# Performance work log

Measured on AMD Instinct MI355X. Metric: run time of the kernel, lower is better.

The kernel has to match this reference:

```python
import jax, jax.numpy as jnp
import numpy as np

N, E = 3072, 49152
C_IN, HID, C_OUT = 16, 64, 3
KS = (2000, 1000, 500)  # ceil(pool_ratio * n_nodes) per depth: 2000/3072, 0.5, 0.5


def gcn(x, A, W, b):
    # GCNConv(improved=True) with edge weights: A_hat = A + 2I,
    # out = D^-1/2 A_hat D^-1/2 (x W) + b
    n = A.shape[0]
    i = jnp.arange(n)
    A_hat = A.at[i, i].add(2.0)
    deg = A_hat.sum(axis=1)
    dis = jnp.where(deg > 0, 1.0 / jnp.sqrt(deg), 0.0)
    return (dis[:, None] * A_hat * dis[None, :]) @ (x @ W) + b


def augment(A):
    # GraphUNet.augment_adj: remove self loops, add self loops (w=1),
    # spspmm(A, A) -> A^2, remove self loops. Dense equivalent.
    n = A.shape[0]
    i = jnp.arange(n)
    A1 = A.at[i, i].set(1.0)
    A2 = A1 @ A1
    return A2.at[i, i].set(0.0)


def topk_pool(x, A, p, k):
    # TopKPooling: score = tanh((x . p)/||p||), keep top-k nodes, scale features
    score = jnp.tanh((x @ p) / jnp.linalg.norm(p))
    _, perm = jax.lax.top_k(score, k)
    x = x[perm] * score[perm][:, None]
    return x, A[perm][:, perm], perm


def setup_inputs():
    key = jax.random.key(0)
    ks = jax.random.split(key, 16)
    g = lambda k, shape, s=1.0: jax.random.normal(k, shape, dtype=jnp.float32) * s
    s = 0.1
    return {
        "x": g(ks[0], (N, C_IN)),
        "edge_index": jax.random.randint(ks[1], (2, E), 0, N),
        "Wd0": g(ks[2], (C_IN, HID), s), "bd0": jnp.zeros((HID,), jnp.float32),
        "Wd1": g(ks[3], (HID, HID), s), "bd1": jnp.zeros((HID,), jnp.float32),
        "Wd2": g(ks[4], (HID, HID), s), "bd2": jnp.zeros((HID,), jnp.float32),
        "Wd3": g(ks[5], (HID, HID), s), "bd3": jnp.zeros((HID,), jnp.float32),
        "p1": g(ks[6], (HID,), s), "p2": g(ks[7], (HID,), s), "p3": g(ks[8], (HID,), s),
        "Wu0": g(ks[9], (HID, HID), s), "bu0": jnp.zeros((HID,), jnp.float32),
        "Wu1": g(ks[10], (HID, HID), s), "bu1": jnp.zeros((HID,), jnp.float32),
        "Wu2": g(ks[11], (HID, C_OUT), s), "bu2": jnp.zeros((C_OUT,), jnp.float32),
    }


def reference(x, edge_index, Wd0, bd0, Wd1, bd1, Wd2, bd2, Wd3, bd3,
              p1, p2, p3, Wu0, bu0, Wu1, bu1, Wu2, bu2):
    # eval mode: dropout_edge(p=0.2) and F.dropout(p=0.92) are identity
    # dense weighted adjacency; duplicate edges sum, matching sparse scatter-add
    A = jnp.zeros((N, N), jnp.float32).at[edge_index[0], edge_index[1]].add(1.0)
    x = jax.nn.relu(gcn(x, A, Wd0, bd0))
    xs, adjs, perms = [x], [A], []
    for i, (W, b, p) in enumerate(((Wd1, bd1, p1), (Wd2, bd2, p2), (Wd3, bd3, p3))):
        A = augment(A)
        x, A, perm = topk_pool(x, A, p, KS[i])
        x = jax.nn.relu(gcn(x, A, W, b))
        if i < 2:
            xs.append(x)
            adjs.append(A)
        perms.append(perm)
    for i, (W, b) in enumerate(((Wu0, bu0), (Wu1, bu1), (Wu2, bu2))):
        j = 2 - i
        res, Aj, perm = xs[j], adjs[j], perms[j]
        up = jnp.zeros_like(res).at[perm].set(x)  # unpool
        x = gcn(res + up, Aj, W, b)  # sum_res=True skip connection
        if i < 2:
            x = jax.nn.relu(x)
    return jax.nn.softmax(x, axis=1)
```

## Files before the change

### kernel.cpp

```cpp
#include <hip/hip_runtime.h>
#include <hip/hip_bf16.h>
#include <cstdint>
#include <cstddef>
#include <math.h>


#define DIVUP(a,b) (((a)+(b)-1)/(b))

using s16x8 = __attribute__((ext_vector_type(8))) short;
using f32x4 = __attribute__((ext_vector_type(4))) float;

template<int N> __device__ __forceinline__ void waitvm() {
    if constexpr (N == 0)       asm volatile("s_waitcnt vmcnt(0)" ::: "memory");
    else if constexpr (N == 4)  asm volatile("s_waitcnt vmcnt(4)" ::: "memory");
    else if constexpr (N == 8)  asm volatile("s_waitcnt vmcnt(8)" ::: "memory");
    else                        asm volatile("s_waitcnt vmcnt(16)" ::: "memory");
}

__device__ __forceinline__ unsigned short f2bf(float v) {
    union { float f; unsigned u; } a; a.f = v;
    unsigned u = a.u;
    u = u + 0x7FFFu + ((u >> 16) & 1u);
    return (unsigned short)(u >> 16);
}
__device__ __forceinline__ float bf2f(unsigned short h) {
    union { unsigned u; float f; } a; a.u = ((unsigned)h) << 16; return a.f;
}
__device__ __forceinline__ unsigned char f2e4m3(float v) {
    if (v <= 0.f) return 0;
    int e = 0; float m = v;
    while (m >= 2.f) { m *= 0.5f; ++e; }
    int mant = (int)(m * 8.f + 0.5f) - 8;
    if (mant >= 8) { mant = 0; ++e; }
    return (unsigned char)(((e + 7) << 3) | mant);
}
__device__ __forceinline__ void gload_lds16(const unsigned short* g, unsigned short* l) {
    __builtin_amdgcn_global_load_lds(
        (const __attribute__((address_space(1))) void*)g,
        (__attribute__((address_space(3))) void*)l, 16, 0, 0);
}
__device__ __forceinline__ void gload_lds16b(const unsigned char* g, unsigned char* l) {
    __builtin_amdgcn_global_load_lds(
        (const __attribute__((address_space(1))) void*)g,
        (__attribute__((address_space(3))) void*)l, 16, 0, 0);
}


__global__ void k_scatter(const int* __restrict__ e, float* __restrict__ A, int E, int n) {
    int t = blockIdx.x * blockDim.x + threadIdx.x;
    if (t < E) atomicAdd(&A[(size_t)e[t] * n + e[E + t]], 1.0f);
}

__global__ void k_a0_plane(const float* __restrict__ A, unsigned short* __restrict__ H,
                           unsigned char* __restrict__ F8,
                           float* __restrict__ d0, float* __restrict__ dsum, int n) {
    int t = blockIdx.x * 256 + threadIdx.x;
    int i = t / n, j = t - i * n;
    float v = A[t];
    if (i == j) { d0[i] = v; v = 1.0f; }
    H[t] = f2bf(v);
    F8[t] = f2e4m3(v);
    __shared__ float red[256];
    red[threadIdx.x] = v; __syncthreads();
    for (int o = 128; o > 0; o >>= 1) {
        if (threadIdx.x < o) red[threadIdx.x] += red[threadIdx.x + o];
        __syncthreads();
    }
    if (threadIdx.x == 0) atomicAdd(&dsum[i], red[0]);
}

__global__ void k_transpose_u8(const unsigned char* __restrict__ S, unsigned char* __restrict__ D, int n) {
    __shared__ unsigned char tile[32][33];
    int bx = blockIdx.x * 32, by = blockIdx.y * 32;
    #pragma unroll
    for (int dy = 0; dy < 32; dy += 8)
        tile[threadIdx.y + dy][threadIdx.x] = S[(size_t)(by + threadIdx.y + dy) * n + bx + threadIdx.x];
    __syncthreads();
    #pragma unroll
    for (int dy = 0; dy < 32; dy += 8)
        D[(size_t)(bx + threadIdx.y + dy) * n + by + threadIdx.x] = tile[threadIdx.x][threadIdx.y + dy];
}

__global__ void k_disv(const float* __restrict__ dsum, const float* __restrict__ diag,
                       float* __restrict__ dis, int n) {
    int i = blockIdx.x * blockDim.x + threadIdx.x;
    if (i >= n) return;
    float deg = dsum[i] + 1.0f + (diag ? diag[i] : 0.0f);
    dis[i] = deg > 0.f ? 1.0f / sqrtf(deg) : 0.f;
}

__global__ void k_disp(const unsigned short* __restrict__ P0, const unsigned short* __restrict__ P1,
                       const unsigned short* __restrict__ P2, int nplanes,
                       float* __restrict__ dis, int np) {
    int i = blockIdx.x;
    const unsigned short* pls[3] = {P0, P1, P2};
    float s = 0.f;
    for (int p = 0; p < nplanes; ++p) {
        const unsigned short* row = pls[p] + (size_t)i * np;
        for (int j = threadIdx.x * 8; j < np; j += 2048) {
            s16x8 v = *(const s16x8*)(row + j);
            #pragma unroll
            for (int e = 0; e < 8; ++e) s += bf2f((unsigned short)v[e]);
        }
    }
    __shared__ float red[256];
    red[threadIdx.x] = s; __syncthreads();
    for (int o = 128; o > 0; o >>= 1) {
        if (threadIdx.x < o) red[threadIdx.x] += red[threadIdx.x + o];
        __syncthreads();
    }
    if (threadIdx.x == 0) dis[i] = 1.0f / sqrtf(red[0] + 1.0f);
}

__global__ void k_scores(const float* __restrict__ x, const float* __restrict__ pv,
                         float* __restrict__ sc, int n) {
    __shared__ float pl[64];
    if (threadIdx.x < 64) pl[threadIdx.x] = pv[threadIdx.x];
    __syncthreads();
    float n2 = 0.f;
    #pragma unroll
    for (int k = 0; k < 64; ++k) n2 += pl[k] * pl[k];
    float nrm = sqrtf(n2);
    int i = blockIdx.x * blockDim.x + threadIdx.x;
    if (i >= n) return;
    const float* xr = x + (size_t)i * 64;
    float d = 0.f;
    #pragma unroll
    for (int k = 0; k < 64; ++k) d += xr[k] * pl[k];
    sc[i] = tanhf(d / nrm);
}

__global__ void k_count_rank(const float* __restrict__ score, int* __restrict__ rank, int n) {
    __shared__ float ls[256];
    const int i = blockIdx.x * 256 + threadIdx.x;
    const int j0 = blockIdx.y * 256;
    int jj_n = n - j0; if (jj_n > 256) jj_n = 256;
    ls[threadIdx.x] = (j0 + threadIdx.x < n) ? score[j0 + threadIdx.x] : -INFINITY;
    __syncthreads();
    if (i >= n) return;
    const float si = score[i];
    int cnt = 0;
    for (int jj = 0; jj < jj_n; ++jj) {
        float sj = ls[jj];
        int j = j0 + jj;
        cnt += (sj > si) || (sj == si && j < i);
    }
    atomicAdd(&rank[i], cnt);
}

__global__ void k_topk_finish(const float* __restrict__ score, const int* __restrict__ rank,
                              const float* __restrict__ x, int n, int k, int kp,
                              int* __restrict__ perm, float* __restrict__ scout,
                              float* __restrict__ xo) {
    int i = blockIdx.x * blockDim.x + threadIdx.x;
    if (i < n) {
        int r = rank[i];
        if (r < k) {
            float s = score[i];
            perm[r] = i; scout[r] = s;
            const float* xr = x + (size_t)i * 64;
            float* xw = xo + (size_t)r * 64;
            #pragma unroll 8
            for (int f = 0; f < 64; ++f) xw[f] = xr[f] * s;
        }
    }
    if (i >= k && i < kp) { perm[i] = 0; scout[i] = 0.f; }
}

__global__ void k_unpool(const float* __restrict__ res, const float* __restrict__ xc,
                         const int* __restrict__ rank, float* __restrict__ o, int n, int k) {
    int t = blockIdx.x * blockDim.x + threadIdx.x;
    if (t >= n * 64) return;
    int r = rank[t >> 6];
    o[t] = res[t] + (r < k ? xc[(size_t)r * 64 + (t & 63)] : 0.f);
}

__global__ void k_xw(const float* __restrict__ x, const float* __restrict__ W,
                     const float* __restrict__ dis, int n, int np, int cin, int ldw, int nout,
                     float* __restrict__ Y, unsigned short* __restrict__ T0,
                     unsigned short* __restrict__ T1, unsigned short* __restrict__ T2) {
    int t = blockIdx.x * blockDim.x + threadIdx.x;
    if (t >= np * 64) return;
    int i = t >> 6, f = t & 63;
    float y = 0.f;
    if (i < n && f < nout) {
        float a = 0.f;
        for (int k = 0; k < cin; ++k) a += x[(size_t)i * cin + k] * W[(size_t)k * ldw + f];
        y = dis[i] * a;
    }
    Y[t] = y;
    unsigned short h0 = f2bf(y);
    float r1 = y - bf2f(h0);
    unsigned short h1 = f2bf(r1);
    float r2 = r1 - bf2f(h1);
    size_t ti = (size_t)f * np + i;
    T0[ti] = h0; T1[ti] = h1; T2[ti] = f2bf(r2);
}


__global__ __launch_bounds__(256) void k_aug8(
    const unsigned char* __restrict__ P8, const unsigned char* __restrict__ Q8,
    const int* __restrict__ perm, int kk, int kp, int K, int ns,
    unsigned short* __restrict__ H0, unsigned short* __restrict__ T0)
{
    constexpr int BM = 128;
    constexpr int PS = 128 * 64;
    constexpr int D = 3;
    constexpr int STG = 2 * PS;
    constexpr int SMEB = (D * STG > 128 * 130 * 2) ? D * STG : 128 * 130 * 2;
    __shared__ __align__(16) unsigned char smem[SMEB];
    const int tid = threadIdx.x, lane = tid & 63;
    const int wm = tid >> 7, wn = (tid >> 6) & 1;
    const int bm = blockIdx.x * BM, bn = blockIdx.y * BM;
    const unsigned char* spA[2];
    const unsigned char* spB[2];
    int dstb[2];
    #pragma unroll
    for (int it = 0; it < 2; ++it) {
        int s = tid + it * 256;
        int row = s >> 2, c = (s & 3) ^ (row & 3);
        dstb[it] = (s - lane) * 16;
        spA[it] = P8 + (size_t)perm[bm + row] * ns + 16 * c;
        spB[it] = Q8 + (size_t)perm[bn + row] * ns + 16 * c;
    }
    f32x4 acc[4][4] = {};
    const int l15 = lane & 15, kb = lane >> 4;
    const int nt = K >> 6;

    auto stage = [&](int b, int koff) {
        unsigned char* base = smem + b * STG;
        #pragma unroll
        for (int it = 0; it < 2; ++it) gload_lds16b(spA[it] + koff, base + dstb[it]);
        #pragma unroll
        for (int it = 0; it < 2; ++it) gload_lds16b(spB[it] + koff, base + PS + dstb[it]);
    };
    auto compute = [&](int b) {
        const unsigned char* base = smem + b * STG;
        #pragma unroll
        for (int h = 0; h < 2; ++h) {
            long av[4], bv[4];
            #pragma unroll
            for (int mi = 0; mi < 4; ++mi) {
                int row = wm * 64 + mi * 16 + l15;
                int slot = (h * 2 + (kb >> 1)) ^ (row & 3);
                av[mi] = *(const long*)(base + row * 64 + slot * 16 + (kb & 1) * 8);
            }
            #pragma unroll
            for (int ni = 0; ni < 4; ++ni) {
                int row = wn * 64 + ni * 16 + l15;
                int slot = (h * 2 + (kb >> 1)) ^ (row & 3);
                bv[ni] = *(const long*)(base + PS + row * 64 + slot * 16 + (kb & 1) * 8);
            }
            #pragma unroll
            for (int mi = 0; mi < 4; ++mi)
                #pragma unroll
                for (int ni = 0; ni < 4; ++ni)
                    acc[mi][ni] = __builtin_amdgcn_mfma_f32_16x16x32_fp8_fp8(
                        av[mi], bv[ni], acc[mi][ni], 0, 0, 0);
        }
    };

    stage(0, 0); stage(1, 64);
    for (int t = 0; t < nt; ++t) {
        const int ahead = nt - 1 - t;
        if (ahead >= D - 1) {
            stage((t + D - 1) % D, (t + D - 1) * 64);
            waitvm<8>();
        } else if (ahead == 1) {
            waitvm<4>();
        } else {
            waitvm<0>();
        }
        __builtin_amdgcn_sched_barrier(0);
        __builtin_amdgcn_s_barrier();
        compute(t % D);
        __builtin_amdgcn_s_barrier();
    }

    const int hi = lane >> 4;
    #pragma unroll
    for (int mi = 0; mi < 4; ++mi)
        #pragma unroll
        for (int ni = 0; ni < 4; ++ni)
            #pragma unroll
            for (int r = 0; r < 4; ++r) {
                int row = bm + wm * 64 + mi * 16 + hi * 4 + r;
                int col = bn + wn * 64 + ni * 16 + l15;
                float v = (row < kk && col < kk) ? ((row == col) ? 1.f : acc[mi][ni][r]) : 0.f;
                H0[(size_t)row * kp + col] = f2bf(v);
            }

    unsigned short* smw = (unsigned short*)smem;
    __syncthreads();
    #pragma unroll
    for (int mi = 0; mi < 4; ++mi)
        #pragma unroll
        for (int ni = 0; ni < 4; ++ni)
            #pragma unroll
            for (int r = 0; r < 4; ++r) {
                int rl = wm * 64 + mi * 16 + hi * 4 + r;
                int cl = wn * 64 + ni * 16 + l15;
                int row = bm + rl, col = bn + cl;
                float v = (row < kk && col < kk) ? ((row == col) ? 1.f : acc[mi][ni][r]) : 0.f;
                smw[rl * 130 + cl] = f2bf(v);
            }
    __syncthreads();
    #pragma unroll
    for (int e = 0; e < 64; ++e) {
        int idx = tid + e * 256;
        int j = idx >> 7, i = idx & 127;
        T0[(size_t)(bn + j) * kp + (bm + i)] = smw[i * 130 + j];
    }
}

template<int TM, int PA, int PB, int NP, int NT>
__global__ __launch_bounds__(256) void k_aug2(
    const unsigned short* __restrict__ Pa, const unsigned short* __restrict__ Pb,
    const unsigned short* __restrict__ Qa, const unsigned short* __restrict__ Qb,
    const int* __restrict__ perm, int kk, int kp, int K, int ns,
    unsigned short* __restrict__ H0, unsigned short* __restrict__ H1,
    unsigned short* __restrict__ H2,
    unsigned short* __restrict__ T0, unsigned short* __restrict__ T1)
{
    constexpr int BM  = TM * 32;
    constexpr int PS  = TM * 2048;
    constexpr int D   = 3;
    constexpr int STG = (PA + PB) * PS;
    constexpr int LPS = TM * (PA + PB);
    constexpr int TRE = NT ? (BM * (BM + 2)) : 0;
    constexpr int SME = (D * STG > TRE) ? (D * STG) : TRE;
    __shared__ __align__(16) unsigned short smem[SME];
    const int tid = threadIdx.x, lane = tid & 63;
    const int wm = tid >> 7, wn = (tid >> 6) & 1;
    const int bm = blockIdx.x * BM, bn = blockIdx.y * BM;
    const unsigned short* P[2] = {Pa, Pb};
    const unsigned short* Q[2] = {Qa, Qb};
    const unsigned short* sp[PA][TM];
    const unsigned short* sq[PB][TM];
    int dst[TM];
    #pragma unroll
    for (int it = 0; it < TM; ++it) {
        int s = tid + it * 256;
        int row = s >> 3, c = (s & 7) ^ (row & 7);
        dst[it] = (s - lane) * 8;
        #pragma unroll
        for (int p = 0; p < PA; ++p)
            sp[p][it] = P[p] + (size_t)perm[bm + row] * ns + 8 * c;
        #pragma unroll
        for (int p = 0; p < PB; ++p)
            sq[p][it] = Q[p] + (size_t)perm[bn + row] * ns + 8 * c;
    }
    f32x4 acc[TM][TM] = {};
    const int l15 = lane & 15, kb = lane >> 4;
    const int nt = K >> 6;

    auto stage = [&](int b, int koff) {
        unsigned short* base = smem + b * STG;
        #pragma unroll
        for (int p = 0; p < PA; ++p)
            #pragma unroll
            for (int it = 0; it < TM; ++it)
                gload_lds16(sp[p][it] + koff, base + p * PS + dst[it]);
        #pragma unroll
        for (int p = 0; p < PB; ++p)
            #pragma unroll
            for (int it = 0; it < TM; ++it)
                gload_lds16(sq[p][it] + koff, base + PA * PS + p * PS + dst[it]);
    };
    auto compute = [&](int b) {
        const unsigned short* base = smem + b * STG;
        #pragma unroll
        for (int h = 0; h < 2; ++h) {
            s16x8 av[PA][TM], bv[PB][TM];
            #pragma unroll
            for (int p = 0; p < PA; ++p)
                #pragma unroll
                for (int mi = 0; mi < TM; ++mi) {
                    int row = wm * (TM * 16) + mi * 16 + l15;
                    int slot = (h * 4 + kb) ^ (row & 7);
                    av[p][mi] = *(const s16x8*)(base + p * PS + row * 64 + slot * 8);
                }
            #pragma unroll
            for (int p = 0; p < PB; ++p)
                #pragma unroll
                for (int ni = 0; ni < TM; ++ni) {
                    int row = wn * (TM * 16) + ni * 16 + l15;
                    int slot = (h * 4 + kb) ^ (row & 7);
                    bv[p][ni] = *(const s16x8*)(base + PA * PS + p * PS + row * 64 + slot * 8);
                }
            #pragma unroll
            for (int mi = 0; mi < TM; ++mi)
                #pragma unroll
                for (int ni = 0; ni < TM; ++ni)
                    #pragma unroll
                    for (int pa = 0; pa < PA; ++pa)
                        #pragma unroll
                        for (int pb = 0; pb < PB; ++pb)
                            acc[mi][ni] = __builtin_amdgcn_mfma_f32_16x16x32_bf16(
                                av[pa][mi], bv[pb][ni], acc[mi][ni], 0, 0, 0);
        }
    };

    for (int i = 0; i < D - 1; ++i) stage(i, i * 64);
    for (int t = 0; t < nt; ++t) {
        const int ahead = nt - 1 - t;
        if (ahead >= D - 1) {
            stage((t + D - 1) % D, (t + D - 1) * 64);
            waitvm<2 * LPS>();
        } else if (ahead == 1) {
            waitvm<LPS>();
        } else {
            waitvm<0>();
        }
        __builtin_amdgcn_sched_barrier(0);
        __builtin_amdgcn_s_barrier();
        compute(t % D);
        __builtin_amdgcn_s_barrier();
    }

    const int hi = lane >> 4;
    #pragma unroll
    for (int mi = 0; mi < TM; ++mi)
        #pragma unroll
        for (int ni = 0; ni < TM; ++ni)
            #pragma unroll
            for (int r = 0; r < 4; ++r) {
                int row = bm + wm * (TM * 16) + mi * 16 + hi * 4 + r;
                int col = bn + wn * (TM * 16) + ni * 16 + l15;
                float v = (row < kk && col < kk) ? ((row == col) ? 1.f : acc[mi][ni][r]) : 0.f;
                unsigned short h0 = f2bf(v);
                size_t o = (size_t)row * kp + col;
                H0[o] = h0;
                if (NP > 1) {
                    float r1 = v - bf2f(h0);
                    unsigned short h1 = f2bf(r1);
                    H1[o] = h1;
                    if (NP > 2) H2[o] = f2bf(r1 - bf2f(h1));
                }
            }

    if (NT > 0) {
        #pragma unroll
        for (int pass = 0; pass < NT; ++pass) {
            __syncthreads();
            #pragma unroll
            for (int mi = 0; mi < TM; ++mi)
                #pragma unroll
                for (int ni = 0; ni < TM; ++ni)
                    #pragma unroll
                    for (int r = 0; r < 4; ++r) {
                        int rl = wm * (TM * 16) + mi * 16 + hi * 4 + r;
                        int cl = wn * (TM * 16) + ni * 16 + l15;
                        int row = bm + rl, col = bn + cl;
                        float v = (row < kk && col < kk) ? ((row == col) ? 1.f : acc[mi][ni][r]) : 0.f;
                        unsigned short h0 = f2bf(v);
                        unsigned short hv = h0;
                        if (pass == 1) hv = f2bf(v - bf2f(h0));
                        smem[rl * (BM + 2) + cl] = hv;
                    }
            __syncthreads();
            unsigned short* T = pass ? T1 : T0;
            #pragma unroll
            for (int e = 0; e < BM * BM / 256; ++e) {
                int idx = tid + e * 256;
                int j = idx / BM, i = idx & (BM - 1);
                T[(size_t)(bn + j) * kp + (bm + i)] = smem[i * (BM + 2) + j];
            }
        }
    }
}

template<int PA>
__global__ __launch_bounds__(256) void k_gcn_gemm(
    const unsigned short* __restrict__ Aa, const unsigned short* __restrict__ Ab,
    const unsigned short* __restrict__ Ac,
    const unsigned short* __restrict__ B0, const unsigned short* __restrict__ B1,
    const unsigned short* __restrict__ B2,
    int np, int kchunk, float* __restrict__ Zp)
{
    __shared__ __align__(16) unsigned short la[PA * 4096];
    __shared__ __align__(16) unsigned short lb[3 * 4096];
    const int tid = threadIdx.x, lane = tid & 63, wv = tid >> 6;
    const int bm = blockIdx.x * 64;
    const int kbeg = blockIdx.y * kchunk;
    const unsigned short* A[3] = {Aa, Ab, Ac};
    const unsigned short* B[3] = {B0, B1, B2};
    const unsigned short* sa[PA][2];
    const unsigned short* sb[3][2];
    int dst[2];
    #pragma unroll
    for (int it = 0; it < 2; ++it) {
        int s = tid + it * 256;
        int row = s >> 3, c = (s & 7) ^ (row & 7);
        dst[it] = (s - lane) * 8;
        #pragma unroll
        for (int p = 0; p < PA; ++p)
            sa[p][it] = A[p] + (size_t)(bm + row) * np + kbeg + 8 * c;
        #pragma unroll
        for (int p = 0; p < 3; ++p)
            sb[p][it] = B[p] + (size_t)row * np + kbeg + 8 * c;
    }
    f32x4 acc[4] = {};
    const int l15 = lane & 15, kb = lane >> 4;
    const int nt = kchunk >> 6;

    for (int tt = 0; tt < nt; ++tt) {
        if (tt) __syncthreads();
        int koff = tt * 64;
        #pragma unroll
        for (int p = 0; p < PA; ++p)
            #pragma unroll
            for (int it = 0; it < 2; ++it)
                gload_lds16(sa[p][it] + koff, &la[p * 4096 + dst[it]]);
        #pragma unroll
        for (int p = 0; p < 3; ++p)
            #pragma unroll
            for (int it = 0; it < 2; ++it)
                gload_lds16(sb[p][it] + koff, &lb[p * 4096 + dst[it]]);
        __syncthreads();
        #pragma unroll
        for (int h = 0; h < 2; ++h) {
            s16x8 av[PA], bv[3][4];
            #pragma unroll
            for (int p = 0; p < PA; ++p) {
                int row = wv * 16 + l15;
                int slot = (h * 4 + kb) ^ (row & 7);
                av[p] = *(const s16x8*)&la[p * 4096 + row * 64 + slot * 8];
            }
            #pragma unroll
            for (int p = 0; p < 3; ++p)
                #pragma unroll
                for (int ni = 0; ni < 4; ++ni) {
                    int row = ni * 16 + l15;
                    int slot = (h * 4 + kb) ^ (row & 7);
                    bv[p][ni] = *(const s16x8*)&lb[p * 4096 + row * 64 + slot * 8];
                }
            #pragma unroll
            for (int ni = 0; ni < 4; ++ni)
                #pragma unroll
                for (int pa = 0; pa < PA; ++pa)
                    #pragma unroll
                    for (int pb = 0; pb <= 2 - pa; ++pb)
                        acc[ni] = __builtin_amdgcn_mfma_f32_16x16x32_bf16(
                            av[pa], bv[pb][ni], acc[ni], 0, 0, 0);
        }
    }

    const int l4 = lane >> 4;
    float* Z = Zp + (size_t)blockIdx.y * np * 64;
    for (int ni = 0; ni < 4; ++ni)
        #pragma unroll
        for (int r = 0; r < 4; ++r) {
            int row = bm + wv * 16 + l4 * 4 + r;
            Z[(size_t)row * 64 + ni * 16 + l15] = acc[ni][r];
        }
}

__global__ void k_gcn_epi(const float* __restrict__ Zp, const float* __restrict__ Y,
                          const float* __restrict__ dis, const float* __restrict__ diagv,
                          const float* __restrict__ b, int n, int np, int nout, int relu,
                          int S, float* __restrict__ xo) {
    int t = blockIdx.x * blockDim.x + threadIdx.x;
    if (t >= n * 64) return;
    int i = t >> 6, f = t & 63;
    float s = 0.f;
    for (int kq = 0; kq < S; ++kq) s += Zp[(size_t)kq * np * 64 + t];
    float coef = 1.f + (diagv ? diagv[i] : 0.f);
    float v = dis[i] * (s + coef * Y[t]) + (f < nout ? b[f] : 0.f);
    if (relu) v = fmaxf(v, 0.f);
    xo[t] = v;
}

__global__ void k_softmax(const float* __restrict__ lg, float* __restrict__ o, int n) {
    int i = blockIdx.x * blockDim.x + threadIdx.x;
    if (i >= n) return;
    float a = lg[i * 64], b = lg[i * 64 + 1], c = lg[i * 64 + 2];
    float m = fmaxf(a, fmaxf(b, c));
    float ea = expf(a - m), eb = expf(b - m), ec = expf(c - m);
    float s = ea + eb + ec;
    o[i * 3] = ea / s; o[i * 3 + 1] = eb / s; o[i * 3 + 2] = ec / s;
}


extern "C" void kernel_launch(void* const* d_in, const int* in_sizes, int n_in,
                              void* d_out, int out_size, void* d_ws, size_t ws_size,
                              hipStream_t stream) {
    const int N0 = 3072;
    const int E = in_sizes[1] / 2;
    const int CIN = in_sizes[0] / N0;

    const float* x_in = (const float*)d_in[0];
    const int*   eidx = (const int*)d_in[1];
    const float* Wd0 = (const float*)d_in[2];  const float* bd0 = (const float*)d_in[3];
    const float* Wd1 = (const float*)d_in[4];  const float* bd1 = (const float*)d_in[5];
    const float* Wd2 = (const float*)d_in[6];  const float* bd2 = (const float*)d_in[7];
    const float* Wd3 = (const float*)d_in[8];  const float* bd3 = (const float*)d_in[9];
    const float* p1  = (const float*)d_in[10]; const float* p2  = (const float*)d_in[11];
    const float* p3  = (const float*)d_in[12];
    const float* Wu0 = (const float*)d_in[13]; const float* bu0 = (const float*)d_in[14];
    const float* Wu1 = (const float*)d_in[15]; const float* bu1 = (const float*)d_in[16];
    const float* Wu2 = (const float*)d_in[17]; const float* bu2 = (const float*)d_in[18];
    float* out = (float*)d_out;

    char* ws = (char*)d_ws;
    size_t off = 0;
    auto alloc = [&](size_t bytes) -> void* {
        off = (off + 255) & ~(size_t)255;
        void* p = ws + off;
        off += bytes;
        return p;
    };

    unsigned short* A0H  = (unsigned short*)alloc((size_t)3072 * 3072 * 2);
    unsigned char*  A0F8 = (unsigned char*)alloc((size_t)3072 * 3072);
    unsigned char*  A0T8 = (unsigned char*)alloc((size_t)3072 * 3072);
    float* d0   = (float*)alloc(3072 * 4);
    float* dis0 = (float*)alloc(3072 * 4);
    float* x0   = (float*)alloc((size_t)3072 * 64 * 4);
    unsigned short* P1H = (unsigned short*)alloc((size_t)2048 * 2048 * 2);
    unsigned short* P1T = (unsigned short*)alloc((size_t)2048 * 2048 * 2);
    float* dis1 = (float*)alloc(2048 * 4);
    float* x1   = (float*)alloc((size_t)2048 * 64 * 4);
    float* xp1  = (float*)alloc((size_t)2048 * 64 * 4);
    unsigned short* P2H  = (unsigned short*)alloc((size_t)1024 * 1024 * 2);
    unsigned short* P2L  = (unsigned short*)alloc((size_t)1024 * 1024 * 2);
    unsigned short* P2TH = (unsigned short*)alloc((size_t)1024 * 1024 * 2);
    unsigned short* P2TL = (unsigned short*)alloc((size_t)1024 * 1024 * 2);
    float* dis2 = (float*)alloc(1024 * 4);
    float* x2   = (float*)alloc((size_t)1024 * 64 * 4);
    float* xp2  = (float*)alloc((size_t)1024 * 64 * 4);
    unsigned short* P3a = (unsigned short*)alloc((size_t)512 * 512 * 2);
    unsigned short* P3b = (unsigned short*)alloc((size_t)512 * 512 * 2);
    unsigned short* P3c = (unsigned short*)alloc((size_t)512 * 512 * 2);
    float* dis3 = (float*)alloc(512 * 4);
    float* x3   = (float*)alloc((size_t)512 * 64 * 4);
    float* xp3  = (float*)alloc((size_t)512 * 64 * 4);
    int*   perm1 = (int*)alloc(2048 * 4);  float* sc1 = (float*)alloc(2048 * 4);
    int*   perm2 = (int*)alloc(1024 * 4);  float* sc2 = (float*)alloc(1024 * 4);
    int*   perm3 = (int*)alloc(512 * 4);   float* sc3 = (float*)alloc(512 * 4);
    float* score = (float*)alloc(3072 * 4);
    float* dsum0 = (float*)alloc(3072 * 4);
    int* rank1 = (int*)alloc(3072 * 4);
    int* rank2 = (int*)alloc(2048 * 4);
    int* rank3 = (int*)alloc(1024 * 4);
    float* Yf  = (float*)alloc((size_t)3072 * 64 * 4);
    unsigned short* Yt0 = (unsigned short*)alloc((size_t)64 * 3072 * 2);
    unsigned short* Yt1 = (unsigned short*)alloc((size_t)64 * 3072 * 2);
    unsigned short* Yt2 = (unsigned short*)alloc((size_t)64 * 3072 * 2);
    float* Zp   = (float*)alloc((size_t)8 * 3072 * 64 * 4);
    float* xlog = (float*)alloc((size_t)3072 * 64 * 4);
    float* t2b  = (float*)alloc((size_t)1024 * 64 * 4);
    float* t1b  = (float*)alloc((size_t)2048 * 64 * 4);
    float* t0b  = (float*)alloc((size_t)3072 * 64 * 4);
    char* scratch = (char*)alloc((size_t)3072 * 3072 * 4);
    if (off > ws_size) return;

    float* A0f = (float*)scratch;

    auto gcn = [&](const float* xin, int cin, const float* W, int ldw, int nout, const float* bias,
                   const unsigned short* Pa, const unsigned short* Pb2, const unsigned short* Pc,
                   int PA, int n, int np2, const float* dis, const float* diagv, int relu, float* xout) {
        k_xw<<<DIVUP(np2 * 64, 256), 256, 0, stream>>>(xin, W, dis, n, np2, cin, ldw, nout, Yf, Yt0, Yt1, Yt2);
        int S = (np2 == 1024) ? 16 : 8;
        int kch = np2 / S;
        dim3 gg(np2 / 64, S);
        if (PA == 1)      k_gcn_gemm<1><<<gg, 256, 0, stream>>>(Pa, Pa, Pa, Yt0, Yt1, Yt2, np2, kch, Zp);
        else if (PA == 2) k_gcn_gemm<2><<<gg, 256, 0, stream>>>(Pa, Pb2, Pb2, Yt0, Yt1, Yt2, np2, kch, Zp);
        else              k_gcn_gemm<3><<<gg, 256, 0, stream>>>(Pa, Pb2, Pc, Yt0, Yt1, Yt2, np2, kch, Zp);
        k_gcn_epi<<<DIVUP(n * 64, 256), 256, 0, stream>>>(Zp, Yf, dis, diagv, bias, n, np2, nout, relu, S, xout);
    };

    auto topk = [&](const float* x, const float* pvec, int n, int k, int kp,
                    int* rank, int* perm, float* scv, float* xo) {
        k_scores<<<DIVUP(n, 256), 256, 0, stream>>>(x, pvec, score, n);
        dim3 gr(DIVUP(n, 256), DIVUP(n, 256));
        k_count_rank<<<gr, 256, 0, stream>>>(score, rank, n);
        k_topk_finish<<<DIVUP(n, 256), 256, 0, stream>>>(score, rank, x, n, k, kp, perm, scv, xo);
    };

    hipMemsetAsync(dsum0, 0, (char*)(rank3 + 1024) - (char*)dsum0, stream);

    hipMemsetAsync(A0f, 0, (size_t)3072 * 3072 * 4, stream);
    k_scatter<<<DIVUP(E, 256), 256, 0, stream>>>(eidx, A0f, E, N0);
    k_a0_plane<<<3072 * 3072 / 256, 256, 0, stream>>>(A0f, A0H, A0F8, d0, dsum0, N0);
    k_transpose_u8<<<dim3(96, 96), dim3(32, 8), 0, stream>>>(A0F8, A0T8, 3072);
    k_disv<<<DIVUP(3072, 256), 256, 0, stream>>>(dsum0, d0, dis0, 3072);

    gcn(x_in, CIN, Wd0, 64, 64, bd0, A0H, A0H, A0H, 1, 3072, 3072, dis0, d0, 1, x0);

    topk(x0, p1, 3072, 2000, 2048, rank1, perm1, sc1, xp1);
    k_aug8<<<dim3(16, 16), 256, 0, stream>>>(
        A0F8, A0T8, perm1, 2000, 2048, 3072, 3072, P1H, P1T);
    k_disp<<<2000, 256, 0, stream>>>(P1H, P1H, P1H, 1, dis1, 2048);
    gcn(xp1, 64, Wd1, 64, 64, bd1, P1H, P1H, P1H, 1, 2000, 2048, dis1, nullptr, 1, x1);

    topk(x1, p2, 2000, 1000, 1024, rank2, perm2, sc2, xp2);
    k_aug2<2, 1, 1, 2, 2><<<dim3(16, 16), 256, 0, stream>>>(
        P1H, P1H, P1T, P1T, perm2, 1000, 1024, 2048, 2048, P2H, P2L, P2L, P2TH, P2TL);
    k_disp<<<1000, 256, 0, stream>>>(P2H, P2L, P2L, 2, dis2, 1024);
    gcn(xp2, 64, Wd2, 64, 64, bd2, P2H, P2L, P2L, 2, 1000, 1024, dis2, nullptr, 1, x2);

    topk(x2, p3, 1000, 500, 512, rank3, perm3, sc3, xp3);
    k_aug2<2, 2, 2, 3, 0><<<dim3(8, 8), 256, 0, stream>>>(
        P2H, P2L, P2TH, P2TL, perm3, 500, 512, 1024, 1024, P3a, P3b, P3c, nullptr, nullptr);
    k_disp<<<500, 256, 0, stream>>>(P3a, P3b, P3c, 3, dis3, 512);
    gcn(xp3, 64, Wd3, 64, 64, bd3, P3a, P3b, P3c, 3, 500, 512, dis3, nullptr, 1, x3);

    k_unpool<<<DIVUP(1000 * 64, 256), 256, 0, stream>>>(x2, x3, rank3, t2b, 1000, 500);
    gcn(t2b, 64, Wu0, 64, 64, bu0, P2H, P2L, P2L, 2, 1000, 1024, dis2, nullptr, 1, xp2);

    k_unpool<<<DIVUP(2000 * 64, 256), 256, 0, stream>>>(x1, xp2, rank2, t1b, 2000, 1000);
    gcn(t1b, 64, Wu1, 64, 64, bu1, P1H, P1H, P1H, 1, 2000, 2048, dis1, nullptr, 1, xp1);

    k_unpool<<<DIVUP(3072 * 64, 256), 256, 0, stream>>>(x0, xp1, rank1, t0b, 3072, 2000);
    gcn(t0b, 64, Wu2, 3, 3, bu2, A0H, A0H, A0H, 1, 3072, 3072, dis0, d0, 0, xlog);

    k_softmax<<<DIVUP(3072, 256), 256, 0, stream>>>(xlog, out, 3072);
}
```

Baseline: 405.8 us.

## Fuse degree sums into augment epilogues and permute fp8 layout for wide LDS reads

The augment GEMM epilogues now reduce each output row across lanes and atomically add it into a per-level degree buffer. This replaces the separate k_disp kernels, which reread the pooled bf16 planes, with the cheap k_disv. The fp8 adjacency and its transpose are stored with a 64-column permutation, so the fp8 GEMM loads one 16-byte vector per row per k-tile instead of two 8-byte loads. The swizzle is adjusted to match, and the transpose now uses 64x64 tiles. Degrees are now summed from unrounded float values, a small numerical change, and the epilogue adds shuffle and atomic work.

```diff
diff --git a/kernel.cpp b/kernel.cpp
--- a/kernel.cpp
+++ b/kernel.cpp
@@ -9,6 +9,7 @@
 
 using s16x8 = __attribute__((ext_vector_type(8))) short;
 using f32x4 = __attribute__((ext_vector_type(4))) float;
+using l64x2 = __attribute__((ext_vector_type(2))) long;
 
 template<int N> __device__ __forceinline__ void waitvm() {
     if constexpr (N == 0)       asm volatile("s_waitcnt vmcnt(0)" ::: "memory");
@@ -33,6 +34,9 @@
     int mant = (int)(m * 8.f + 0.5f) - 8;
     if (mant >= 8) { mant = 0; ++e; }
     return (unsigned char)(((e + 7) << 3) | mant);
+}
+__device__ __forceinline__ int perm64(int x) {
+    return ((x >> 3) & 3) * 16 + ((x >> 5) & 1) * 8 + (x & 7);
 }
 __device__ __forceinline__ void gload_lds16(const unsigned short* g, unsigned short* l) {
     __builtin_amdgcn_global_load_lds(
@@ -59,7 +63,7 @@
     float v = A[t];
     if (i == j) { d0[i] = v; v = 1.0f; }
     H[t] = f2bf(v);
-    F8[t] = f2e4m3(v);
+    F8[(size_t)i * n + (j & ~63) + perm64(j & 63)] = f2e4m3(v);
     __shared__ float red[256];
     red[threadIdx.x] = v; __syncthreads();
     for (int o = 128; o > 0; o >>= 1) {
@@ -69,16 +73,17 @@
     if (threadIdx.x == 0) atomicAdd(&dsum[i], red[0]);
 }
 
-__global__ void k_transpose_u8(const unsigned char* __restrict__ S, unsigned char* __restrict__ D, int n) {
-    __shared__ unsigned char tile[32][33];
-    int bx = blockIdx.x * 32, by = blockIdx.y * 32;
-    #pragma unroll
-    for (int dy = 0; dy < 32; dy += 8)
-        tile[threadIdx.y + dy][threadIdx.x] = S[(size_t)(by + threadIdx.y + dy) * n + bx + threadIdx.x];
+__global__ void k_transpose_i8(const unsigned char* __restrict__ S, unsigned char* __restrict__ D, int n) {
+    __shared__ unsigned char tile[64][65];
+    int bx = blockIdx.x * 64, by = blockIdx.y * 64;
+    const int tx = threadIdx.x & 63, ty = threadIdx.x >> 6;
+    #pragma unroll
+    for (int dy = 0; dy < 64; dy += 4)
+        tile[ty + dy][tx] = S[(size_t)(by + ty + dy) * n + bx + perm64(tx)];
     __syncthreads();
     #pragma unroll
-    for (int dy = 0; dy < 32; dy += 8)
-        D[(size_t)(bx + threadIdx.y + dy) * n + by + threadIdx.x] = tile[threadIdx.x][threadIdx.y + dy];
+    for (int dy = 0; dy < 64; dy += 4)
+        D[(size_t)(bx + ty + dy) * n + by + perm64(tx)] = tile[tx][ty + dy];
 }
 
 __global__ void k_disv(const float* __restrict__ dsum, const float* __restrict__ diag,
@@ -87,29 +92,6 @@
     if (i >= n) return;
     float deg = dsum[i] + 1.0f + (diag ? diag[i] : 0.0f);
     dis[i] = deg > 0.f ? 1.0f / sqrtf(deg) : 0.f;
-}
-
-__global__ void k_disp(const unsigned short* __restrict__ P0, const unsigned short* __restrict__ P1,
-                       const unsigned short* __restrict__ P2, int nplanes,
-                       float* __restrict__ dis, int np) {
-    int i = blockIdx.x;
-    const unsigned short* pls[3] = {P0, P1, P2};
-    float s = 0.f;
-    for (int p = 0; p < nplanes; ++p) {
-        const unsigned short* row = pls[p] + (size_t)i * np;
-        for (int j = threadIdx.x * 8; j < np; j += 2048) {
-            s16x8 v = *(const s16x8*)(row + j);
-            #pragma unroll
-            for (int e = 0; e < 8; ++e) s += bf2f((unsigned short)v[e]);
-        }
-    }
-    __shared__ float red[256];
-    red[threadIdx.x] = s; __syncthreads();
-    for (int o = 128; o > 0; o >>= 1) {
-        if (threadIdx.x < o) red[threadIdx.x] += red[threadIdx.x + o];
-        __syncthreads();
-    }
-    if (threadIdx.x == 0) dis[i] = 1.0f / sqrtf(red[0] + 1.0f);
 }
 
 __global__ void k_scores(const float* __restrict__ x, const float* __restrict__ pv,
@@ -201,9 +183,9 @@
 __global__ __launch_bounds__(256) void k_aug8(
     const unsigned char* __restrict__ P8, const unsigned char* __restrict__ Q8,
     const int* __restrict__ perm, int kk, int kp, int K, int ns,
-    unsigned short* __restrict__ H0, unsigned short* __restrict__ T0)
+    unsigned short* __restrict__ H0, unsigned short* __restrict__ T0,
+    float* __restrict__ dsum)
 {
-    constexpr int BM = 128;
     constexpr int PS = 128 * 64;
     constexpr int D = 3;
     constexpr int STG = 2 * PS;
@@ -211,14 +193,14 @@
     __shared__ __align__(16) unsigned char smem[SMEB];
     const int tid = threadIdx.x, lane = tid & 63;
     const int wm = tid >> 7, wn = (tid >> 6) & 1;
-    const int bm = blockIdx.x * BM, bn = blockIdx.y * BM;
+    const int bm = blockIdx.x * 128, bn = blockIdx.y * 128;
     const unsigned char* spA[2];
     const unsigned char* spB[2];
     int dstb[2];
     #pragma unroll
     for (int it = 0; it < 2; ++it) {
         int s = tid + it * 256;
-        int row = s >> 2, c = (s & 3) ^ (row & 3);
+        int row = s >> 2, c = (s & 3) ^ ((row >> 1) & 3);
         dstb[it] = (s - lane) * 16;
         spA[it] = P8 + (size_t)perm[bm + row] * ns + 16 * c;
         spB[it] = Q8 + (size_t)perm[bn + row] * ns + 16 * c;
@@ -236,28 +218,27 @@
     };
     auto compute = [&](int b) {
         const unsigned char* base = smem + b * STG;
-        #pragma unroll
-        for (int h = 0; h < 2; ++h) {
-            long av[4], bv[4];
-            #pragma unroll
-            for (int mi = 0; mi < 4; ++mi) {
-                int row = wm * 64 + mi * 16 + l15;
-                int slot = (h * 2 + (kb >> 1)) ^ (row & 3);
-                av[mi] = *(const long*)(base + row * 64 + slot * 16 + (kb & 1) * 8);
-            }
-            #pragma unroll
-            for (int ni = 0; ni < 4; ++ni) {
-                int row = wn * 64 + ni * 16 + l15;
-                int slot = (h * 2 + (kb >> 1)) ^ (row & 3);
-                bv[ni] = *(const long*)(base + PS + row * 64 + slot * 16 + (kb & 1) * 8);
-            }
+        l64x2 av[4], bv[4];
+        #pragma unroll
+        for (int mi = 0; mi < 4; ++mi) {
+            int row = wm * 64 + mi * 16 + l15;
+            int slot = kb ^ ((row >> 1) & 3);
+            av[mi] = *(const l64x2*)(base + row * 64 + slot * 16);
+        }
+        #pragma unroll
+        for (int ni = 0; ni < 4; ++ni) {
+            int row = wn * 64 + ni * 16 + l15;
+            int slot = kb ^ ((row >> 1) & 3);
+            bv[ni] = *(const l64x2*)(base + PS + row * 64 + slot * 16);
+        }
+        #pragma unroll
+        for (int h = 0; h < 2; ++h)
             #pragma unroll
             for (int mi = 0; mi < 4; ++mi)
                 #pragma unroll
                 for (int ni = 0; ni < 4; ++ni)
                     acc[mi][ni] = __builtin_amdgcn_mfma_f32_16x16x32_fp8_fp8(
-                        av[mi], bv[ni], acc[mi][ni], 0, 0, 0);
-        }
+                        av[mi][h], bv[ni][h], acc[mi][ni], 0, 0, 0);
     };
 
     stage(0, 0); stage(1, 64);
@@ -281,14 +262,20 @@
     #pragma unroll
     for (int mi = 0; mi < 4; ++mi)
         #pragma unroll
-        for (int ni = 0; ni < 4; ++ni)
-            #pragma unroll
-            for (int r = 0; r < 4; ++r) {
-                int row = bm + wm * 64 + mi * 16 + hi * 4 + r;
+        for (int r = 0; r < 4; ++r) {
+            int row = bm + wm * 64 + mi * 16 + hi * 4 + r;
+            float s = 0.f;
+            #pragma unroll
+            for (int ni = 0; ni < 4; ++ni) {
                 int col = bn + wn * 64 + ni * 16 + l15;
                 float v = (row < kk && col < kk) ? ((row == col) ? 1.f : acc[mi][ni][r]) : 0.f;
                 H0[(size_t)row * kp + col] = f2bf(v);
+                s += v;
             }
+            #pragma unroll
+            for (int m = 1; m < 16; m <<= 1) s += __shfl_xor(s, m);
+            if (l15 == 0) atomicAdd(&dsum[row], s);
+        }
 
     unsigned short* smw = (unsigned short*)smem;
     __syncthreads();
@@ -320,7 +307,8 @@
     const int* __restrict__ perm, int kk, int kp, int K, int ns,
     unsigned short* __restrict__ H0, unsigned short* __restrict__ H1,
     unsigned short* __restrict__ H2,
-    unsigned short* __restrict__ T0, unsigned short* __restrict__ T1)
+    unsigned short* __restrict__ T0, unsigned short* __restrict__ T1,
+    float* __restrict__ dsum)
 {
     constexpr int BM  = TM * 32;
     constexpr int PS  = TM * 2048;
@@ -422,12 +410,14 @@
     #pragma unroll
     for (int mi = 0; mi < TM; ++mi)
         #pragma unroll
-        for (int ni = 0; ni < TM; ++ni)
-            #pragma unroll
-            for (int r = 0; r < 4; ++r) {
-                int row = bm + wm * (TM * 16) + mi * 16 + hi * 4 + r;
+        for (int r = 0; r < 4; ++r) {
+            int row = bm + wm * (TM * 16) + mi * 16 + hi * 4 + r;
+            float s = 0.f;
+            #pragma unroll
+            for (int ni = 0; ni < TM; ++ni) {
                 int col = bn + wn * (TM * 16) + ni * 16 + l15;
                 float v = (row < kk && col < kk) ? ((row == col) ? 1.f : acc[mi][ni][r]) : 0.f;
+                s += v;
                 unsigned short h0 = f2bf(v);
                 size_t o = (size_t)row * kp + col;
                 H0[o] = h0;
@@ -438,6 +428,10 @@
                     if (NP > 2) H2[o] = f2bf(r1 - bf2f(h1));
                 }
             }
+            #pragma unroll
+            for (int m = 1; m < 16; m <<= 1) s += __shfl_xor(s, m);
+            if (l15 == 0) atomicAdd(&dsum[row], s);
+        }
 
     if (NT > 0) {
         #pragma unroll
@@ -640,6 +634,9 @@
     int*   perm3 = (int*)alloc(512 * 4);   float* sc3 = (float*)alloc(512 * 4);
     float* score = (float*)alloc(3072 * 4);
     float* dsum0 = (float*)alloc(3072 * 4);
+    float* dsum1 = (float*)alloc(2048 * 4);
+    float* dsum2 = (float*)alloc(1024 * 4);
+    float* dsum3 = (float*)alloc(512 * 4);
     int* rank1 = (int*)alloc(3072 * 4);
     int* rank2 = (int*)alloc(2048 * 4);
     int* rank3 = (int*)alloc(1024 * 4);
@@ -683,27 +680,27 @@
     hipMemsetAsync(A0f, 0, (size_t)3072 * 3072 * 4, stream);
     k_scatter<<<DIVUP(E, 256), 256, 0, stream>>>(eidx, A0f, E, N0);
     k_a0_plane<<<3072 * 3072 / 256, 256, 0, stream>>>(A0f, A0H, A0F8, d0, dsum0, N0);
-    k_transpose_u8<<<dim3(96, 96), dim3(32, 8), 0, stream>>>(A0F8, A0T8, 3072);
+    k_transpose_i8<<<dim3(48, 48), 256, 0, stream>>>(A0F8, A0T8, 3072);
     k_disv<<<DIVUP(3072, 256), 256, 0, stream>>>(dsum0, d0, dis0, 3072);
 
     gcn(x_in, CIN, Wd0, 64, 64, bd0, A0H, A0H, A0H, 1, 3072, 3072, dis0, d0, 1, x0);
 
     topk(x0, p1, 3072, 2000, 2048, rank1, perm1, sc1, xp1);
     k_aug8<<<dim3(16, 16), 256, 0, stream>>>(
-        A0F8, A0T8, perm1, 2000, 2048, 3072, 3072, P1H, P1T);
-    k_disp<<<2000, 256, 0, stream>>>(P1H, P1H, P1H, 1, dis1, 2048);
+        A0F8, A0T8, perm1, 2000, 2048, 3072, 3072, P1H, P1T, dsum1);
+    k_disv<<<DIVUP(2048, 256), 256, 0, stream>>>(dsum1, nullptr, dis1, 2048);
     gcn(xp1, 64, Wd1, 64, 64, bd1, P1H, P1H, P1H, 1, 2000, 2048, dis1, nullptr, 1, x1);
 
     topk(x1, p2, 2000, 1000, 1024, rank2, perm2, sc2, xp2);
     k_aug2<2, 1, 1, 2, 2><<<dim3(16, 16), 256, 0, stream>>>(
-        P1H, P1H, P1T, P1T, perm2, 1000, 1024, 2048, 2048, P2H, P2L, P2L, P2TH, P2TL);
-    k_disp<<<1000, 256, 0, stream>>>(P2H, P2L, P2L, 2, dis2, 1024);
+        P1H, P1H, P1T, P1T, perm2, 1000, 1024, 2048, 2048, P2H, P2L, P2L, P2TH, P2TL, dsum2);
+    k_disv<<<DIVUP(1024, 256), 256, 0, stream>>>(dsum2, nullptr, dis2, 1024);
     gcn(xp2, 64, Wd2, 64, 64, bd2, P2H, P2L, P2L, 2, 1000, 1024, dis2, nullptr, 1, x2);
 
     topk(x2, p3, 1000, 500, 512, rank3, perm3, sc3, xp3);
     k_aug2<2, 2, 2, 3, 0><<<dim3(8, 8), 256, 0, stream>>>(
-        P2H, P2L, P2TH, P2TL, perm3, 500, 512, 1024, 1024, P3a, P3b, P3c, nullptr, nullptr);
-    k_disp<<<500, 256, 0, stream>>>(P3a, P3b, P3c, 3, dis3, 512);
+        P2H, P2L, P2TH, P2TL, perm3, 500, 512, 1024, 1024, P3a, P3b, P3c, nullptr, nullptr, dsum3);
+    k_disv<<<DIVUP(512, 256), 256, 0, stream>>>(dsum3, nullptr, dis3, 512);
     gcn(xp3, 64, Wd3, 64, 64, bd3, P3a, P3b, P3c, 3, 500, 512, dis3, nullptr, 1, x3);
 
     k_unpool<<<DIVUP(1000 * 64, 256), 256, 0, stream>>>(x2, x3, rank3, t2b, 1000, 500);
```

Result: faster. 393.3 us (-3.1%).
